# Kernel optimization log

Measured on AMD Instinct MI355X. Metric: run time of the kernel, lower is better.

Reference implementation:

```python
import jax, jax.numpy as jnp
import numpy as np

B, S, D, HD = 16, 2048, 1024, 64  # batch, seq, n_embd, head_dim


def setup_inputs() -> dict:
    key = jax.random.key(0)
    ks = jax.random.split(key, 4)
    std = 1.0 / np.sqrt(D)
    return {
        "x": jax.random.normal(ks[0], (B, S, D), dtype=jnp.float32),
        "Wq": jax.random.normal(ks[1], (D, HD), dtype=jnp.float32) * std,
        "bq": jnp.zeros((HD,), dtype=jnp.float32),
        "Wk": jax.random.normal(ks[2], (D, HD), dtype=jnp.float32) * std,
        "bk": jnp.zeros((HD,), dtype=jnp.float32),
        "Wv": jax.random.normal(ks[3], (D, HD), dtype=jnp.float32) * std,
        "bv": jnp.zeros((HD,), dtype=jnp.float32),
    }


def reference(x, Wq, bq, Wk, bk, Wv, bv):
    q = x @ Wq + bq  # [B,S,HD]
    k = x @ Wk + bk
    v = x @ Wv + bv
    scale = jnp.asarray(HD, x.dtype) ** -0.5
    scores = jnp.einsum("bqd,bkd->bqk", q, k) * scale  # [B,S,S]
    seq = x.shape[1]
    causal = jnp.tril(jnp.ones((seq, seq), dtype=bool))  # True = keep
    scores = jnp.where(causal, scores, jnp.asarray(-jnp.inf, scores.dtype))
    probs = jax.nn.softmax(scores, axis=-1)
    return jnp.einsum("bqk,bkd->bqd", probs, v)  # [B,S,HD]
```

## Files before the change

### kernel.cpp

```cpp
#include <hip/hip_runtime.h>
#include <hip/hip_bf16.h>
#include <math.h>

constexpr int Bsz  = 16;
constexpr int Seq  = 2048;
constexpr int Din  = 1024;
constexpr int Hd   = 64;
constexpr int Rows = Bsz * Seq;

typedef short  short8 __attribute__((ext_vector_type(8)));
typedef short  sh4    __attribute__((ext_vector_type(4)));
typedef float  f32x4  __attribute__((ext_vector_type(4)));

__device__ __forceinline__ short bf16_bits(float f) {
    __hip_bfloat16 h = __float2bfloat16(f);
    return __builtin_bit_cast(short, h);
}

__global__ __launch_bounds__(256) void wt_prep(
    const float* __restrict__ Wq, const float* __restrict__ Wk,
    const float* __restrict__ Wv, short* __restrict__ Wf)
{
    const int u     = blockIdx.x * 256 + threadIdx.x;
    const int chunk = u / 768;
    const int rem   = u - chunk * 768;
    const int f     = rem >> 6;
    const int lane  = rem & 63;
    const int wg    = f >> 2, nt = f & 3;
    const int quad  = lane >> 4, l16 = lane & 15;
    const float* W  = (wg == 0) ? Wq : (wg == 1) ? Wk : Wv;
    const int k0 = chunk * 32 + quad * 8;
    const int n  = nt * 16 + l16;
    short8 v;
    #pragma unroll
    for (int j = 0; j < 8; ++j) v[j] = bf16_bits(W[(size_t)(k0 + j) * Hd + n]);
    *(short8*)(Wf + (size_t)u * 8) = v;
}

__global__ __launch_bounds__(512, 4) void qkv_kernel(
    const float* __restrict__ x,
    const short* __restrict__ Wf,
    const float* __restrict__ bq, const float* __restrict__ bk,
    const float* __restrict__ bv,
    short* __restrict__ Qf, short* __restrict__ Kf, short* __restrict__ Vf)
{
    const int tid  = threadIdx.x;
    const int wave = tid >> 6;
    const int lane = tid & 63;
    const int quad = lane >> 4;
    const int l16  = lane & 15;
    const int g    = wave >> 2;
    const int w    = wave & 3;
    const int m0   = blockIdx.x * 64;

    __shared__ __align__(16) short Xs[2][64 * 40];
    __shared__ __align__(16) short Bs[2][6144];
    __shared__ __align__(16) short epi[64 * 200];
    __shared__ __align__(16) short epiV[64 * 80];

    const int srow = tid >> 3;
    const int sgrp = tid & 7;
    const float* xsrc = x + (size_t)(m0 + srow) * Din + sgrp * 4;

    f32x4 acc[6] = {};

    auto stage = [&](int c, int bufi) {
        const float4 xv = *(const float4*)(xsrc + c * 32);
        const short* wsrc = Wf + (size_t)c * 6144 + wave * 512 + lane * 8;
        const short8 w0 = *(const short8*)wsrc;
        sh4 sv;
        sv[0] = bf16_bits(xv.x); sv[1] = bf16_bits(xv.y);
        sv[2] = bf16_bits(xv.z); sv[3] = bf16_bits(xv.w);
        *(sh4*)&Xs[bufi][srow * 40 + sgrp * 4] = sv;
        *(short8*)&Bs[bufi][wave * 512 + lane * 8] = w0;
        if (wave < 4) {
            const short8 w1 = *(const short8*)(wsrc + 4096);
            *(short8*)&Bs[bufi][(wave + 8) * 512 + lane * 8] = w1;
        }
    };

    stage(0, 0);
    __syncthreads();
    for (int c = 0; c < 32; ++c) {
        const int cur = c & 1;
        if (c + 1 < 32) stage(c + 1, cur ^ 1);
        const short8 a = *(const short8*)&Xs[cur][(w * 16 + l16) * 40 + quad * 8];
        #pragma unroll
        for (int fi = 0; fi < 6; ++fi) {
            const short8 bb = *(const short8*)&Bs[cur][(g * 6 + fi) * 512 + lane * 8];
            acc[fi] = __builtin_amdgcn_mfma_f32_16x16x32_bf16(a, bb, acc[fi], 0, 0, 0);
        }
        __syncthreads();
    }

    const float* bias_all[3] = {bq, bk, bv};
    #pragma unroll
    for (int fi = 0; fi < 6; ++fi) {
        const int f  = g * 6 + fi;
        const int wg = f >> 2, nt = f & 3;
        const float bb = bias_all[wg][nt * 16 + l16];
        #pragma unroll
        for (int r = 0; r < 4; ++r) {
            const short v = bf16_bits(acc[fi][r] + bb);
            const int row = w * 16 + quad * 4 + r;
            epi[row * 200 + wg * 64 + nt * 16 + l16] = v;
            if (wg == 2) epiV[(nt * 16 + l16) * 80 + row] = v;
        }
    }
    __syncthreads();
    {
        const int lane2 = tid & 63;
        const int q16 = lane2 & 15, q4 = lane2 >> 4;
        {
            const int tg_l = tid >> 7, dh = (tid >> 6) & 1;
            const short8 v = *(const short8*)&epi[(tg_l * 16 + q16) * 200 + dh * 32 + q4 * 8];
            *(short8*)(Qf + (((size_t)(blockIdx.x * 4 + tg_l) * 2 + dh) * 64 + lane2) * 8) = v;
        }
        {
            const int dh = tid >> 8, nt = (tid >> 6) & 3;
            const short8 v = *(const short8*)&epi[(nt * 16 + q16) * 200 + 64 + dh * 32 + q4 * 8];
            *(short8*)(Kf + ((((size_t)blockIdx.x * 2 + dh) * 4 + nt) * 64 + lane2) * 8) = v;
        }
        {
            const int th = tid >> 8, nt = (tid >> 6) & 3;
            const short8 v = *(const short8*)&epiV[(nt * 16 + q16) * 80 + th * 32 + q4 * 8];
            *(short8*)(Vf + ((((size_t)blockIdx.x * 2 + th) * 4 + nt) * 64 + lane2) * 8) = v;
        }
    }
}

__global__ __launch_bounds__(256) void attn_kernel(
    const short* __restrict__ Qf, const short* __restrict__ Kf,
    const short* __restrict__ Vf, float* __restrict__ out)
{
    const int tid  = threadIdx.x;
    const int wave = tid >> 6;
    const int lane = tid & 63;
    const int quad = lane >> 4;
    const int l16  = lane & 15;
    const int b    = blockIdx.y;
    const int bx   = blockIdx.x;
    const int qt   = (bx & 1) ? (31 - (bx >> 1)) : (bx >> 1);
    const int q0   = qt * 64;

    __shared__ __align__(16) short Ps[4][16 * 72];

    const int tgq = b * 128 + qt * 4 + wave;
    const short8 qf0 = *(const short8*)(Qf + ((size_t)tgq * 2 + 0) * 512 + lane * 8);
    const short8 qf1 = *(const short8*)(Qf + ((size_t)tgq * 2 + 1) * 512 + lane * 8);

    f32x4 o[4] = {};
    float m_run[4], l_run[4];
    #pragma unroll
    for (int r = 0; r < 4; ++r) { m_run[r] = -INFINITY; l_run[r] = 0.0f; }

    const float C = 0.125f * 1.44269504088896340736f;

    for (int kt = 0; kt <= qt; ++kt) {
        const short* ktile = Kf + (size_t)(b * 32 + kt) * 4096;
        const short* vtile = Vf + (size_t)(b * 32 + kt) * 4096;

        f32x4 s[4] = {};
        #pragma unroll
        for (int nt = 0; nt < 4; ++nt) {
            const short8 kf0 = *(const short8*)(ktile + ((0 * 4 + nt) * 64 + lane) * 8);
            const short8 kf1 = *(const short8*)(ktile + ((1 * 4 + nt) * 64 + lane) * 8);
            s[nt] = __builtin_amdgcn_mfma_f32_16x16x32_bf16(qf0, kf0, s[nt], 0, 0, 0);
            s[nt] = __builtin_amdgcn_mfma_f32_16x16x32_bf16(qf1, kf1, s[nt], 0, 0, 0);
        }

        if (kt == qt) {
            #pragma unroll
            for (int nt = 0; nt < 4; ++nt) {
                const int kg = nt * 16 + l16;
                #pragma unroll
                for (int r = 0; r < 4; ++r) {
                    const int qg = wave * 16 + quad * 4 + r;
                    s[nt][r] = (kg <= qg) ? s[nt][r] * C : -INFINITY;
                }
            }
        } else {
            #pragma unroll
            for (int nt = 0; nt < 4; ++nt)
                #pragma unroll
                for (int r = 0; r < 4; ++r) s[nt][r] *= C;
        }

        float rm[4];
        #pragma unroll
        for (int r = 0; r < 4; ++r)
            rm[r] = fmaxf(fmaxf(s[0][r], s[1][r]), fmaxf(s[2][r], s[3][r]));
        #pragma unroll
        for (int off = 1; off < 16; off <<= 1)
            #pragma unroll
            for (int r = 0; r < 4; ++r)
                rm[r] = fmaxf(rm[r], __shfl_xor(rm[r], off));

        float alpha[4];
        #pragma unroll
        for (int r = 0; r < 4; ++r) {
            const float mn = fmaxf(m_run[r], rm[r]);
            alpha[r] = exp2f(m_run[r] - mn);
            m_run[r] = mn;
        }

        float rs[4] = {0.f, 0.f, 0.f, 0.f};
        #pragma unroll
        for (int nt = 0; nt < 4; ++nt)
            #pragma unroll
            for (int r = 0; r < 4; ++r) {
                const float p = exp2f(s[nt][r] - m_run[r]);
                s[nt][r] = p;
                rs[r] += p;
            }
        #pragma unroll
        for (int off = 1; off < 16; off <<= 1)
            #pragma unroll
            for (int r = 0; r < 4; ++r)
                rs[r] += __shfl_xor(rs[r], off);
        #pragma unroll
        for (int r = 0; r < 4; ++r) l_run[r] = l_run[r] * alpha[r] + rs[r];

        #pragma unroll
        for (int r = 0; r < 4; ++r) {
            o[0][r] *= alpha[r]; o[1][r] *= alpha[r];
            o[2][r] *= alpha[r]; o[3][r] *= alpha[r];
        }

        #pragma unroll
        for (int nt = 0; nt < 4; ++nt)
            #pragma unroll
            for (int r = 0; r < 4; ++r)
                Ps[wave][(quad * 4 + r) * 72 + nt * 16 + l16] = bf16_bits(s[nt][r]);

        const short8 pf0 = *(const short8*)&Ps[wave][l16 * 72 + quad * 8];
        const short8 pf1 = *(const short8*)&Ps[wave][l16 * 72 + 32 + quad * 8];

        #pragma unroll
        for (int nt = 0; nt < 4; ++nt) {
            const short8 vA = *(const short8*)(vtile + ((0 * 4 + nt) * 64 + lane) * 8);
            const short8 vB = *(const short8*)(vtile + ((1 * 4 + nt) * 64 + lane) * 8);
            o[nt] = __builtin_amdgcn_mfma_f32_16x16x32_bf16(pf0, vA, o[nt], 0, 0, 0);
            o[nt] = __builtin_amdgcn_mfma_f32_16x16x32_bf16(pf1, vB, o[nt], 0, 0, 0);
        }
    }

    float inv[4];
    #pragma unroll
    for (int r = 0; r < 4; ++r) inv[r] = 1.0f / l_run[r];
    const size_t obase = ((size_t)b * Seq + q0 + wave * 16 + quad * 4) * Hd + l16;
    #pragma unroll
    for (int r = 0; r < 4; ++r) {
        out[obase + (size_t)r * Hd +  0] = o[0][r] * inv[r];
        out[obase + (size_t)r * Hd + 16] = o[1][r] * inv[r];
        out[obase + (size_t)r * Hd + 32] = o[2][r] * inv[r];
        out[obase + (size_t)r * Hd + 48] = o[3][r] * inv[r];
    }
}

extern "C" void kernel_launch(void* const* d_in, const int* in_sizes, int n_in,
                              void* d_out, int out_size, void* d_ws, size_t ws_size,
                              hipStream_t stream)
{
    const float* x  = (const float*)d_in[0];
    const float* Wq = (const float*)d_in[1];
    const float* bq = (const float*)d_in[2];
    const float* Wk = (const float*)d_in[3];
    const float* bk = (const float*)d_in[4];
    const float* Wv = (const float*)d_in[5];
    const float* bv = (const float*)d_in[6];
    float* out = (float*)d_out;

    short* Qf = (short*)d_ws;
    short* Kf = Qf + (size_t)Rows * Hd;
    short* Vf = Kf + (size_t)Rows * Hd;
    short* Wf = Vf + (size_t)Rows * Hd;

    wt_prep<<<96, 256, 0, stream>>>(Wq, Wk, Wv, Wf);
    qkv_kernel<<<512, 512, 0, stream>>>(x, Wf, bq, bk, bv, Qf, Kf, Vf);
    attn_kernel<<<dim3(32, 16), 256, 0, stream>>>(Qf, Kf, Vf, out);
}
```

Before: 321.2 us.

## Split attention KV tiles across waves and drop LDS staging in QKV GEMM

The attention kernel now gives each block one 16-row query slice. Its four waves take interleaved KV tiles (split-K), and their partial max, sum and output are merged through shared memory at the end. The grid grows fourfold, which is meant to raise occupancy and balance work across the causal triangle. The QKV projection kernel drops its double-buffered LDS staging and block-wide syncs: each wave reads x and the prepacked weights straight from global memory and computes all 12 fragments. The risks are the extra reduction epilogue in attention, redundant global weight loads per wave, and higher register pressure from 12 accumulators.

```diff
diff --git a/kernel.cpp b/kernel.cpp
--- a/kernel.cpp
+++ b/kernel.cpp
@@ -9,7 +9,6 @@
 constexpr int Rows = Bsz * Seq;
 
 typedef short  short8 __attribute__((ext_vector_type(8)));
-typedef short  sh4    __attribute__((ext_vector_type(4)));
 typedef float  f32x4  __attribute__((ext_vector_type(4)));
 
 __device__ __forceinline__ short bf16_bits(float f) {
@@ -37,7 +36,7 @@
     *(short8*)(Wf + (size_t)u * 8) = v;
 }
 
-__global__ __launch_bounds__(512, 4) void qkv_kernel(
+__global__ __launch_bounds__(256) void qkv_kernel(
     const float* __restrict__ x,
     const short* __restrict__ Wf,
     const float* __restrict__ bq, const float* __restrict__ bk,
@@ -49,83 +48,77 @@
     const int lane = tid & 63;
     const int quad = lane >> 4;
     const int l16  = lane & 15;
-    const int g    = wave >> 2;
-    const int w    = wave & 3;
-    const int m0   = blockIdx.x * 64;
-
-    __shared__ __align__(16) short Xs[2][64 * 40];
-    __shared__ __align__(16) short Bs[2][6144];
-    __shared__ __align__(16) short epi[64 * 200];
-    __shared__ __align__(16) short epiV[64 * 80];
-
-    const int srow = tid >> 3;
-    const int sgrp = tid & 7;
-    const float* xsrc = x + (size_t)(m0 + srow) * Din + sgrp * 4;
-
-    f32x4 acc[6] = {};
-
-    auto stage = [&](int c, int bufi) {
-        const float4 xv = *(const float4*)(xsrc + c * 32);
-        const short* wsrc = Wf + (size_t)c * 6144 + wave * 512 + lane * 8;
-        const short8 w0 = *(const short8*)wsrc;
-        sh4 sv;
-        sv[0] = bf16_bits(xv.x); sv[1] = bf16_bits(xv.y);
-        sv[2] = bf16_bits(xv.z); sv[3] = bf16_bits(xv.w);
-        *(sh4*)&Xs[bufi][srow * 40 + sgrp * 4] = sv;
-        *(short8*)&Bs[bufi][wave * 512 + lane * 8] = w0;
-        if (wave < 4) {
-            const short8 w1 = *(const short8*)(wsrc + 4096);
-            *(short8*)&Bs[bufi][(wave + 8) * 512 + lane * 8] = w1;
-        }
-    };
-
-    stage(0, 0);
+    const int bx   = blockIdx.x;
+    const int m0   = bx * 64;
+
+    const float* xrow = x + (size_t)(m0 + wave * 16 + l16) * Din + quad * 8;
+
+    f32x4 acc[12] = {};
+
+    #pragma unroll 2
+    for (int c = 0; c < 32; ++c) {
+        const float4 a0 = *(const float4*)(xrow + c * 32);
+        const float4 a1 = *(const float4*)(xrow + c * 32 + 4);
+        short8 af;
+        af[0] = bf16_bits(a0.x); af[1] = bf16_bits(a0.y);
+        af[2] = bf16_bits(a0.z); af[3] = bf16_bits(a0.w);
+        af[4] = bf16_bits(a1.x); af[5] = bf16_bits(a1.y);
+        af[6] = bf16_bits(a1.z); af[7] = bf16_bits(a1.w);
+        const short* wsrc = Wf + (size_t)c * 6144 + lane * 8;
+        #pragma unroll
+        for (int f = 0; f < 12; ++f) {
+            const short8 bb = *(const short8*)(wsrc + f * 512);
+            acc[f] = __builtin_amdgcn_mfma_f32_16x16x32_bf16(af, bb, acc[f], 0, 0, 0);
+        }
+    }
+
+    __shared__ __align__(16) short eS[4][2][16 * 72];
+    __shared__ __align__(16) short eV[64 * 80];
+
+    #pragma unroll
+    for (int wg = 0; wg < 2; ++wg) {
+        const float* bias = wg ? bk : bq;
+        #pragma unroll
+        for (int nt = 0; nt < 4; ++nt) {
+            const float bb = bias[nt * 16 + l16];
+            #pragma unroll
+            for (int r = 0; r < 4; ++r)
+                eS[wave][wg][(quad * 4 + r) * 72 + nt * 16 + l16] =
+                    bf16_bits(acc[wg * 4 + nt][r] + bb);
+        }
+    }
+    #pragma unroll
+    for (int wg = 0; wg < 2; ++wg) {
+        const short8 v0 = *(const short8*)&eS[wave][wg][l16 * 72 + quad * 8];
+        const short8 v1 = *(const short8*)&eS[wave][wg][l16 * 72 + 32 + quad * 8];
+        if (wg == 0) {
+            const size_t tg = (size_t)bx * 4 + wave;
+            *(short8*)(Qf + (tg * 2 + 0) * 512 + lane * 8) = v0;
+            *(short8*)(Qf + (tg * 2 + 1) * 512 + lane * 8) = v1;
+        } else {
+            *(short8*)(Kf + (((size_t)bx * 2 + 0) * 4 + wave) * 512 + lane * 8) = v0;
+            *(short8*)(Kf + (((size_t)bx * 2 + 1) * 4 + wave) * 512 + lane * 8) = v1;
+        }
+    }
+
+    #pragma unroll
+    for (int nt = 0; nt < 4; ++nt) {
+        const float bb = bv[nt * 16 + l16];
+        #pragma unroll
+        for (int r = 0; r < 4; ++r)
+            eV[(nt * 16 + l16) * 80 + wave * 16 + quad * 4 + r] =
+                bf16_bits(acc[8 + nt][r] + bb);
+    }
     __syncthreads();
-    for (int c = 0; c < 32; ++c) {
-        const int cur = c & 1;
-        if (c + 1 < 32) stage(c + 1, cur ^ 1);
-        const short8 a = *(const short8*)&Xs[cur][(w * 16 + l16) * 40 + quad * 8];
-        #pragma unroll
-        for (int fi = 0; fi < 6; ++fi) {
-            const short8 bb = *(const short8*)&Bs[cur][(g * 6 + fi) * 512 + lane * 8];
-            acc[fi] = __builtin_amdgcn_mfma_f32_16x16x32_bf16(a, bb, acc[fi], 0, 0, 0);
-        }
-        __syncthreads();
-    }
-
-    const float* bias_all[3] = {bq, bk, bv};
-    #pragma unroll
-    for (int fi = 0; fi < 6; ++fi) {
-        const int f  = g * 6 + fi;
-        const int wg = f >> 2, nt = f & 3;
-        const float bb = bias_all[wg][nt * 16 + l16];
-        #pragma unroll
-        for (int r = 0; r < 4; ++r) {
-            const short v = bf16_bits(acc[fi][r] + bb);
-            const int row = w * 16 + quad * 4 + r;
-            epi[row * 200 + wg * 64 + nt * 16 + l16] = v;
-            if (wg == 2) epiV[(nt * 16 + l16) * 80 + row] = v;
-        }
-    }
-    __syncthreads();
-    {
-        const int lane2 = tid & 63;
-        const int q16 = lane2 & 15, q4 = lane2 >> 4;
-        {
-            const int tg_l = tid >> 7, dh = (tid >> 6) & 1;
-            const short8 v = *(const short8*)&epi[(tg_l * 16 + q16) * 200 + dh * 32 + q4 * 8];
-            *(short8*)(Qf + (((size_t)(blockIdx.x * 4 + tg_l) * 2 + dh) * 64 + lane2) * 8) = v;
-        }
-        {
-            const int dh = tid >> 8, nt = (tid >> 6) & 3;
-            const short8 v = *(const short8*)&epi[(nt * 16 + q16) * 200 + 64 + dh * 32 + q4 * 8];
-            *(short8*)(Kf + ((((size_t)blockIdx.x * 2 + dh) * 4 + nt) * 64 + lane2) * 8) = v;
-        }
-        {
-            const int th = tid >> 8, nt = (tid >> 6) & 3;
-            const short8 v = *(const short8*)&epiV[(nt * 16 + q16) * 80 + th * 32 + q4 * 8];
-            *(short8*)(Vf + ((((size_t)blockIdx.x * 2 + th) * 4 + nt) * 64 + lane2) * 8) = v;
-        }
+    #pragma unroll
+    for (int s = 0; s < 2; ++s) {
+        const int slot   = tid + s * 256;
+        const int lane_s = slot & 63;
+        const int u      = slot >> 6;
+        const int th     = u >> 2, ntd = u & 3;
+        const int q_s    = lane_s >> 4, l_s = lane_s & 15;
+        const short8 v = *(const short8*)&eV[(ntd * 16 + l_s) * 80 + th * 32 + q_s * 8];
+        *(short8*)(Vf + (((size_t)bx * 2 + th) * 4 + ntd) * 512 + lane_s * 8) = v;
     }
 }
 
@@ -140,14 +133,20 @@
     const int l16  = lane & 15;
     const int b    = blockIdx.y;
     const int bx   = blockIdx.x;
-    const int qt   = (bx & 1) ? (31 - (bx >> 1)) : (bx >> 1);
-    const int q0   = qt * 64;
-
-    __shared__ __align__(16) short Ps[4][16 * 72];
-
-    const int tgq = b * 128 + qt * 4 + wave;
-    const short8 qf0 = *(const short8*)(Qf + ((size_t)tgq * 2 + 0) * 512 + lane * 8);
-    const short8 qf1 = *(const short8*)(Qf + ((size_t)tgq * 2 + 1) * 512 + lane * 8);
+    const int qs   = (bx & 1) ? (127 - (bx >> 1)) : (bx >> 1);
+    const int dTile = qs >> 2;
+    const int tiles = dTile + 1;
+    const int qoff  = (qs & 3) * 16;
+
+    __shared__ __align__(16) unsigned char sm[17408 + 512];
+    short* Ps   = (short*)sm;
+    float* Obuf = (float*)sm;
+    float* mb   = (float*)(sm + 17408);
+    float* lb   = mb + 64;
+
+    const size_t tg = (size_t)b * 128 + qs;
+    const short8 qf0 = *(const short8*)(Qf + (tg * 2 + 0) * 512 + lane * 8);
+    const short8 qf1 = *(const short8*)(Qf + (tg * 2 + 1) * 512 + lane * 8);
 
     f32x4 o[4] = {};
     float m_run[4], l_run[4];
@@ -156,7 +155,7 @@
 
     const float C = 0.125f * 1.44269504088896340736f;
 
-    for (int kt = 0; kt <= qt; ++kt) {
+    for (int kt = wave; kt < tiles; kt += 4) {
         const short* ktile = Kf + (size_t)(b * 32 + kt) * 4096;
         const short* vtile = Vf + (size_t)(b * 32 + kt) * 4096;
 
@@ -169,13 +168,13 @@
             s[nt] = __builtin_amdgcn_mfma_f32_16x16x32_bf16(qf1, kf1, s[nt], 0, 0, 0);
         }
 
-        if (kt == qt) {
+        if (kt == dTile) {
             #pragma unroll
             for (int nt = 0; nt < 4; ++nt) {
                 const int kg = nt * 16 + l16;
                 #pragma unroll
                 for (int r = 0; r < 4; ++r) {
-                    const int qg = wave * 16 + quad * 4 + r;
+                    const int qg = qoff + quad * 4 + r;
                     s[nt][r] = (kg <= qg) ? s[nt][r] * C : -INFINITY;
                 }
             }
@@ -231,10 +230,10 @@
         for (int nt = 0; nt < 4; ++nt)
             #pragma unroll
             for (int r = 0; r < 4; ++r)
-                Ps[wave][(quad * 4 + r) * 72 + nt * 16 + l16] = bf16_bits(s[nt][r]);
-
-        const short8 pf0 = *(const short8*)&Ps[wave][l16 * 72 + quad * 8];
-        const short8 pf1 = *(const short8*)&Ps[wave][l16 * 72 + 32 + quad * 8];
+                Ps[wave * 1152 + (quad * 4 + r) * 72 + nt * 16 + l16] = bf16_bits(s[nt][r]);
+
+        const short8 pf0 = *(const short8*)&Ps[wave * 1152 + l16 * 72 + quad * 8];
+        const short8 pf1 = *(const short8*)&Ps[wave * 1152 + l16 * 72 + 32 + quad * 8];
 
         #pragma unroll
         for (int nt = 0; nt < 4; ++nt) {
@@ -245,16 +244,44 @@
         }
     }
 
-    float inv[4];
-    #pragma unroll
-    for (int r = 0; r < 4; ++r) inv[r] = 1.0f / l_run[r];
-    const size_t obase = ((size_t)b * Seq + q0 + wave * 16 + quad * 4) * Hd + l16;
+    if (l16 == 0) {
+        #pragma unroll
+        for (int r = 0; r < 4; ++r) mb[wave * 16 + quad * 4 + r] = m_run[r];
+    }
+    __syncthreads();
+
+    float fac[4];
     #pragma unroll
     for (int r = 0; r < 4; ++r) {
-        out[obase + (size_t)r * Hd +  0] = o[0][r] * inv[r];
-        out[obase + (size_t)r * Hd + 16] = o[1][r] * inv[r];
-        out[obase + (size_t)r * Hd + 32] = o[2][r] * inv[r];
-        out[obase + (size_t)r * Hd + 48] = o[3][r] * inv[r];
+        const int row = quad * 4 + r;
+        const float mg = fmaxf(fmaxf(mb[row], mb[16 + row]),
+                               fmaxf(mb[32 + row], mb[48 + row]));
+        fac[r] = exp2f(m_run[r] - mg);
+    }
+    if (l16 == 0) {
+        #pragma unroll
+        for (int r = 0; r < 4; ++r) lb[wave * 16 + quad * 4 + r] = l_run[r] * fac[r];
+    }
+    #pragma unroll
+    for (int nt = 0; nt < 4; ++nt)
+        #pragma unroll
+        for (int r = 0; r < 4; ++r)
+            Obuf[wave * 1088 + (quad * 4 + r) * 68 + nt * 16 + l16] = o[nt][r] * fac[r];
+    __syncthreads();
+
+    {
+        const int row = tid >> 4;
+        const int c0  = (tid & 15) * 4;
+        const float lsum = lb[row] + lb[16 + row] + lb[32 + row] + lb[48 + row];
+        float4 a = *(const float4*)&Obuf[0 * 1088 + row * 68 + c0];
+        const float4 a1 = *(const float4*)&Obuf[1 * 1088 + row * 68 + c0];
+        const float4 a2 = *(const float4*)&Obuf[2 * 1088 + row * 68 + c0];
+        const float4 a3 = *(const float4*)&Obuf[3 * 1088 + row * 68 + c0];
+        a.x += a1.x + a2.x + a3.x;  a.y += a1.y + a2.y + a3.y;
+        a.z += a1.z + a2.z + a3.z;  a.w += a1.w + a2.w + a3.w;
+        const float inv = 1.0f / lsum;
+        float4 r4 = make_float4(a.x * inv, a.y * inv, a.z * inv, a.w * inv);
+        *(float4*)(out + ((size_t)b * Seq + qs * 16 + row) * Hd + c0) = r4;
     }
 }
 
@@ -277,6 +304,6 @@
     short* Wf = Vf + (size_t)Rows * Hd;
 
     wt_prep<<<96, 256, 0, stream>>>(Wq, Wk, Wv, Wf);
-    qkv_kernel<<<512, 512, 0, stream>>>(x, Wf, bq, bk, bv, Qf, Kf, Vf);
-    attn_kernel<<<dim3(32, 16), 256, 0, stream>>>(Qf, Kf, Vf, out);
-}
+    qkv_kernel<<<512, 256, 0, stream>>>(x, Wf, bq, bk, bv, Qf, Kf, Vf);
+    attn_kernel<<<dim3(128, 16), 256, 0, stream>>>(Qf, Kf, Vf, out);
+}
```

After: 291.3 us. 9.3% less time.
